# Performance work log

Hardware: AMD Instinct MI355X
Metric: run time of the kernel (lower is better)

## Reference

```python
import jax, jax.numpy as jnp
import numpy as np

N_NODES = 100000
N_EDGES = 1600000
IN_DIM, HID_DIM, OUT_DIM = 128, 128, 64


def setup_inputs() -> dict:
    key = jax.random.key(0)
    k1, k2, k3, k4, k5 = jax.random.split(key, 5)
    x = jax.random.normal(k1, (N_NODES, IN_DIM), dtype=jnp.float32)
    edge_index = jax.random.randint(k2, (2, N_EDGES), 0, N_NODES, dtype=jnp.int64)
    # PyG GCNConv linear weights (no bias); Glorot-ish scale for stability
    W1 = jax.random.normal(k3, (IN_DIM, HID_DIM), dtype=jnp.float32) * 0.05
    W2 = jax.random.normal(k4, (HID_DIM, HID_DIM), dtype=jnp.float32) * 0.05
    W3 = jax.random.normal(k5, (HID_DIM, OUT_DIM), dtype=jnp.float32) * 0.05
    return {"x": x, "edge_index": edge_index, "W1": W1, "W2": W2, "W3": W3}


def _gcn_conv(h, W, src, dst, num_nodes):
    # GCNConv(add_self_loops=False, normalize=False, bias=False):
    # linear transform, then scatter-add messages from src into dst
    msg = jnp.take(h @ W, src, axis=0)          # [E, d_out] gather
    return jax.ops.segment_sum(msg, dst, num_segments=num_nodes)  # [N, d_out]


def reference(x, edge_index, W1, W2, W3):
    num_nodes = x.shape[0]
    src, dst = edge_index[0], edge_index[1]
    h = jax.nn.relu(_gcn_conv(x, W1, src, dst, num_nodes))
    # dropout p=0.0 / eval mode -> identity
    h = jax.nn.relu(_gcn_conv(h, W2, src, dst, num_nodes))
    out = _gcn_conv(h, W3, src, dst, num_nodes)
    return jax.nn.log_softmax(out, axis=1)
```

## Files before the change

### kernel.cpp

```cpp
#include <hip/hip_runtime.h>
#include <hip/hip_bf16.h>

#define KDIM 128

typedef __attribute__((ext_vector_type(8))) __bf16 bf16x8;
typedef __attribute__((ext_vector_type(4))) float f32x4;
typedef __attribute__((ext_vector_type(2))) float f32x2;

static __device__ __forceinline__ unsigned short f2bf(float f) {
  unsigned u = __float_as_uint(f);
  u += 0x7fffu + ((u >> 16) & 1u);
  return (unsigned short)(u >> 16);
}
static __device__ __forceinline__ unsigned pack_bf16x2(float a, float b) {
  return (unsigned)f2bf(a) | ((unsigned)f2bf(b) << 16);
}
static __device__ __forceinline__ float2 unpack_bf16x2(unsigned u) {
  return make_float2(__uint_as_float(u << 16), __uint_as_float(u & 0xffff0000u));
}
static __device__ __forceinline__ unsigned relu2(unsigned u) {
  unsigned r = u;
  if (u & 0x00008000u) r &= 0xffff0000u;
  if (u & 0x80000000u) r &= 0x0000ffffu;
  return r;
}

static __device__ __forceinline__ unsigned char f2fp8(float f) {
#if __has_builtin(__builtin_amdgcn_cvt_pk_fp8_f32)
  return (unsigned char)(__builtin_amdgcn_cvt_pk_fp8_f32(f, f, 0, false) & 0xff);
#else
  unsigned s = (__float_as_uint(f) >> 24) & 0x80u;
  float a = fminf(fabsf(f), 448.f);
  if (a < 0.015625f) {
    unsigned m = (unsigned)(a * 512.f + 0.5f);
    return (unsigned char)(s | m);
  }
  unsigned v = __float_as_uint(a);
  v += 0x7ffffu + ((v >> 20) & 1u);
  unsigned em = (v >> 20) - 960u;
  if (em > 0x7eu) em = 0x7eu;
  return (unsigned char)(s | em);
#endif
}
static __device__ __forceinline__ float fp8dec(unsigned b) {
  unsigned s = (b & 0x80u) << 24;
  unsigned em = b & 0x7fu;
  float mag = (em >= 8) ? __uint_as_float((em + 960u) << 20)
                        : (float)em * 0.001953125f;
  return __uint_as_float(__float_as_uint(mag) | s);
}
static __device__ __forceinline__ float4 fp8x4_to_f32(unsigned u) {
#if __has_builtin(__builtin_amdgcn_cvt_pk_f32_fp8)
  f32x2 lo = __builtin_amdgcn_cvt_pk_f32_fp8(u, false);
  f32x2 hi = __builtin_amdgcn_cvt_pk_f32_fp8(u, true);
  return make_float4(lo[0], lo[1], hi[0], hi[1]);
#else
  return make_float4(fp8dec(u & 255u), fp8dec((u >> 8) & 255u),
                     fp8dec((u >> 16) & 255u), fp8dec(u >> 24));
#endif
}

__global__ __launch_bounds__(256) void wtrans_k(const float* __restrict__ W,
                                                unsigned short* __restrict__ Wt,
                                                int NOUT) {
  const int t = blockIdx.x * 256 + threadIdx.x;
  if (t >= NOUT * KDIM) return;
  const int n = t >> 7;
  const int k = t & 127;
  Wt[t] = f2bf(W[k * NOUT + n]);
}

template<int NOUT, bool AF32, bool RELU>
__global__ __launch_bounds__(512) void gemm_mfma_k(const void* __restrict__ Av,
                                                   const unsigned short* __restrict__ Wt,
                                                   unsigned char* __restrict__ C, int M) {
  constexpr int NT = NOUT / 16;
  __shared__ unsigned short Ws[NOUT][136];

  const int tid = threadIdx.x;
  for (int i = tid; i < NOUT * 16; i += 512) {
    const int n = i >> 4, k8 = i & 15;
    const uint4 v = *reinterpret_cast<const uint4*>(&Wt[n * KDIM + k8 * 8]);
    *reinterpret_cast<uint4*>(&Ws[n][k8 * 8]) = v;
  }

  const int wv = tid >> 6;
  const int l  = tid & 63;
  const int am = l & 15;
  const int kb = l >> 4;
  const int arow_g = blockIdx.x * 128 + wv * 16 + am;
  const bool valid = arow_g < M;
  const int arow = valid ? arow_g : 0;

  uint4 afr[4];
  if constexpr (AF32) {
    const float* A = (const float*)Av;
    #pragma unroll
    for (int ks = 0; ks < 4; ++ks) {
      const float4 lo = *reinterpret_cast<const float4*>(&A[(size_t)arow * 128 + ks * 32 + kb * 8]);
      const float4 hi = *reinterpret_cast<const float4*>(&A[(size_t)arow * 128 + ks * 32 + kb * 8 + 4]);
      afr[ks] = make_uint4(pack_bf16x2(lo.x, lo.y), pack_bf16x2(lo.z, lo.w),
                           pack_bf16x2(hi.x, hi.y), pack_bf16x2(hi.z, hi.w));
    }
  } else {
    const unsigned* A = (const unsigned*)Av;
    #pragma unroll
    for (int ks = 0; ks < 4; ++ks) {
      uint4 u = *reinterpret_cast<const uint4*>(&A[(size_t)arow * 64 + ks * 16 + kb * 4]);
      if constexpr (RELU) {
        u.x = relu2(u.x); u.y = relu2(u.y); u.z = relu2(u.z); u.w = relu2(u.w);
      }
      afr[ks] = u;
    }
  }
  if (!valid) {
    afr[0] = make_uint4(0, 0, 0, 0); afr[1] = afr[0];
    afr[2] = afr[0];                 afr[3] = afr[0];
  }

  f32x4 acc[NT];
  #pragma unroll
  for (int nt = 0; nt < NT; ++nt) {
    acc[nt][0] = 0.f; acc[nt][1] = 0.f; acc[nt][2] = 0.f; acc[nt][3] = 0.f;
  }

  __syncthreads();
  #pragma unroll
  for (int ks = 0; ks < 4; ++ks) {
    const bf16x8 a = __builtin_bit_cast(bf16x8, afr[ks]);
    #pragma unroll
    for (int nt = 0; nt < NT; ++nt) {
      const uint4 bv = *reinterpret_cast<const uint4*>(&Ws[nt * 16 + am][ks * 32 + kb * 8]);
      acc[nt] = __builtin_amdgcn_mfma_f32_16x16x32_bf16(
          a, __builtin_bit_cast(bf16x8, bv), acc[nt], 0, 0, 0);
    }
  }

  const int crow0 = blockIdx.x * 128 + wv * 16 + kb * 4;
  #pragma unroll
  for (int nt = 0; nt < NT; ++nt) {
    #pragma unroll
    for (int r = 0; r < 4; ++r) {
      const int rr = crow0 + r;
      if (rr < M) C[(size_t)rr * NOUT + nt * 16 + am] = f2fp8(acc[nt][r]);
    }
  }
}

__global__ __launch_bounds__(512) void hist_k(const int* __restrict__ dst,
                                              int* __restrict__ histT, int E) {
  __shared__ int h[256];
  if (threadIdx.x < 256) h[threadIdx.x] = 0;
  __syncthreads();
  for (int e = blockIdx.x * 512 + threadIdx.x; e < E; e += 256 * 512)
    atomicAdd(&h[dst[e] >> 9], 1);
  __syncthreads();
  if (threadIdx.x < 256) histT[threadIdx.x * 256 + blockIdx.x] = h[threadIdx.x];
}

__global__ __launch_bounds__(256) void scan1_k(const int* __restrict__ in,
                                               int* __restrict__ out,
                                               int* __restrict__ bsum, int N) {
  __shared__ int ls[256];
  const int t = threadIdx.x;
  const int base = blockIdx.x * 2048 + t * 8;
  int v[8];
  if (base + 8 <= N) {
    *reinterpret_cast<int4*>(&v[0]) = *reinterpret_cast<const int4*>(&in[base]);
    *reinterpret_cast<int4*>(&v[4]) = *reinterpret_cast<const int4*>(&in[base + 4]);
  } else {
    #pragma unroll
    for (int j = 0; j < 8; ++j) v[j] = (base + j < N) ? in[base + j] : 0;
  }
  int s = 0;
  #pragma unroll
  for (int j = 0; j < 8; ++j) { const int tmp = v[j]; v[j] = s; s += tmp; }
  int x = s;
  ls[t] = x;
  __syncthreads();
  for (int off = 1; off < 256; off <<= 1) {
    int y = 0;
    if (t >= off) y = ls[t - off];
    __syncthreads();
    x += y;
    ls[t] = x;
    __syncthreads();
  }
  const int excl = x - s;
  #pragma unroll
  for (int j = 0; j < 8; ++j)
    if (base + j < N) out[base + j] = excl + v[j];
  if (t == 255) bsum[blockIdx.x] = x;
}

__global__ __launch_bounds__(64) void scan2_k(const int* __restrict__ bsum,
                                              int* __restrict__ bscan, int NB) {
  const int t = threadIdx.x;
  const int v = (t < NB) ? bsum[t] : 0;
  int x = v;
  #pragma unroll
  for (int off = 1; off < 64; off <<= 1) {
    const int y = __shfl_up(x, off, 64);
    if (t >= off) x += y;
  }
  bscan[t] = x - v;
}

__global__ __launch_bounds__(256) void addoff_k(int* __restrict__ off,
                                                const int* __restrict__ bscan) {
  const int i = blockIdx.x * 256 + threadIdx.x;
  off[i] += bscan[i >> 11];
}

__global__ __launch_bounds__(512) void binscatter_k(const int* __restrict__ src,
                                                    const int* __restrict__ dst,
                                                    const int* __restrict__ histOff,
                                                    unsigned long long* __restrict__ epack,
                                                    int E) {
  __shared__ int cur[256];
  if (threadIdx.x < 256) cur[threadIdx.x] = histOff[threadIdx.x * 256 + blockIdx.x];
  __syncthreads();
  for (int e = blockIdx.x * 512 + threadIdx.x; e < E; e += 256 * 512) {
    const int d = dst[e], s = src[e];
    const int pos = atomicAdd(&cur[d >> 9], 1);
    epack[pos] = ((unsigned long long)(unsigned)d << 32) | (unsigned)s;
  }
}

__global__ __launch_bounds__(512) void binsort_k(const unsigned long long* __restrict__ epack,
                                                 const int* __restrict__ histOff,
                                                 int* __restrict__ rowptr,
                                                 int* __restrict__ col,
                                                 int N, int E) {
  __shared__ int hist[512];
  __shared__ int ls[256];
  __shared__ int cur[512];
  const int b = blockIdx.x;
  const int t = threadIdx.x;
  const int nbins = (N + 511) >> 9;
  const int beg = histOff[b * 256];
  const int end = (b + 1 < nbins) ? histOff[(b + 1) * 256] : E;

  hist[t] = 0;
  __syncthreads();
  for (int j = beg + t; j < end; j += 512)
    atomicAdd(&hist[(int)(epack[j] >> 32) & 511], 1);
  __syncthreads();

  int a = 0, b2 = 0, x = 0;
  if (t < 256) { a = hist[2 * t]; b2 = hist[2 * t + 1]; x = a + b2; ls[t] = x; }
  __syncthreads();
  for (int off = 1; off < 256; off <<= 1) {
    int y = 0;
    if (t < 256 && t >= off) y = ls[t - off];
    __syncthreads();
    if (t < 256) { x += y; ls[t] = x; }
    __syncthreads();
  }
  if (t < 256) {
    const int excl = x - a - b2;
    cur[2 * t] = excl;
    cur[2 * t + 1] = excl + a;
    const int g0 = b * 512 + 2 * t;
    if (g0 <= N) rowptr[g0] = beg + excl;
    if (g0 + 1 <= N) rowptr[g0 + 1] = beg + excl + a;
  }
  __syncthreads();
  for (int j = beg + t; j < end; j += 512) {
    const unsigned long long p = epack[j];
    const int d = (int)(p >> 32) & 511;
    const int s = (int)(p & 0xffffffffu);
    const int pos = atomicAdd(&cur[d], 1);
    col[beg + pos] = s;
  }
}

__global__ __launch_bounds__(256) void gather128_k(const unsigned* __restrict__ H32,
                                                   const int* __restrict__ rowptr,
                                                   const int* __restrict__ col,
                                                   unsigned* __restrict__ out, int N) {
  const int w = (int)((blockIdx.x * 256u + threadIdx.x) >> 6);
  const int lane = threadIdx.x & 63;
  const int h = lane >> 5;
  const int l5 = lane & 31;
  if (w >= N) return;
  const int beg = __builtin_amdgcn_readfirstlane(rowptr[w]);
  const int end = __builtin_amdgcn_readfirstlane(rowptr[w + 1]);

  float4 acc0 = make_float4(0.f, 0.f, 0.f, 0.f);
  float4 acc1 = make_float4(0.f, 0.f, 0.f, 0.f);
  float4 acc2 = make_float4(0.f, 0.f, 0.f, 0.f);
  float4 acc3 = make_float4(0.f, 0.f, 0.f, 0.f);

  int e = beg;
  for (; e + 8 <= end; e += 8) {
    const int sA = col[e + h];
    const int sB = col[e + 2 + h];
    const int sC = col[e + 4 + h];
    const int sD = col[e + 6 + h];
    const unsigned uA = H32[(size_t)sA * 32 + l5];
    const unsigned uB = H32[(size_t)sB * 32 + l5];
    const unsigned uC = H32[(size_t)sC * 32 + l5];
    const unsigned uD = H32[(size_t)sD * 32 + l5];
    const float4 vA = fp8x4_to_f32(uA), vB = fp8x4_to_f32(uB);
    const float4 vC = fp8x4_to_f32(uC), vD = fp8x4_to_f32(uD);
    acc0.x += vA.x; acc0.y += vA.y; acc0.z += vA.z; acc0.w += vA.w;
    acc1.x += vB.x; acc1.y += vB.y; acc1.z += vB.z; acc1.w += vB.w;
    acc2.x += vC.x; acc2.y += vC.y; acc2.z += vC.z; acc2.w += vC.w;
    acc3.x += vD.x; acc3.y += vD.y; acc3.z += vD.z; acc3.w += vD.w;
  }
  for (; e + 2 <= end; e += 2) {
    const float4 v = fp8x4_to_f32(H32[(size_t)col[e + h] * 32 + l5]);
    acc0.x += v.x; acc0.y += v.y; acc0.z += v.z; acc0.w += v.w;
  }
  if (e < end && h == 0) {
    const float4 v = fp8x4_to_f32(H32[(size_t)col[e] * 32 + l5]);
    acc1.x += v.x; acc1.y += v.y; acc1.z += v.z; acc1.w += v.w;
  }

  float4 a;
  a.x = (acc0.x + acc1.x) + (acc2.x + acc3.x);
  a.y = (acc0.y + acc1.y) + (acc2.y + acc3.y);
  a.z = (acc0.z + acc1.z) + (acc2.z + acc3.z);
  a.w = (acc0.w + acc1.w) + (acc2.w + acc3.w);
  a.x += __shfl_xor(a.x, 32, 64);
  a.y += __shfl_xor(a.y, 32, 64);
  a.z += __shfl_xor(a.z, 32, 64);
  a.w += __shfl_xor(a.w, 32, 64);

  if (h == 0) {
    *reinterpret_cast<uint2*>(&out[(size_t)w * 64 + l5 * 2]) =
        make_uint2(pack_bf16x2(a.x, a.y), pack_bf16x2(a.z, a.w));
  }
}

__global__ __launch_bounds__(256) void gather64lsm_k(const unsigned* __restrict__ H32,
                                                     const int* __restrict__ rowptr,
                                                     const int* __restrict__ col,
                                                     float* __restrict__ out, int N) {
  const int w = (int)((blockIdx.x * 256u + threadIdx.x) >> 6);
  const int lane = threadIdx.x & 63;
  const int q = lane >> 4;
  const int l4 = lane & 15;
  if (w >= N) return;
  const int beg = __builtin_amdgcn_readfirstlane(rowptr[w]);
  const int end = __builtin_amdgcn_readfirstlane(rowptr[w + 1]);

  float4 acc0 = make_float4(0.f, 0.f, 0.f, 0.f);
  float4 acc1 = make_float4(0.f, 0.f, 0.f, 0.f);

  int e = beg;
  for (; e + 8 <= end; e += 8) {
    const int s0 = col[e + q];
    const int s1 = col[e + 4 + q];
    const float4 v0 = fp8x4_to_f32(H32[(size_t)s0 * 16 + l4]);
    const float4 v1 = fp8x4_to_f32(H32[(size_t)s1 * 16 + l4]);
    acc0.x += v0.x; acc0.y += v0.y; acc0.z += v0.z; acc0.w += v0.w;
    acc1.x += v1.x; acc1.y += v1.y; acc1.z += v1.z; acc1.w += v1.w;
  }
  if (e + 4 <= end) {
    const float4 v = fp8x4_to_f32(H32[(size_t)col[e + q] * 16 + l4]);
    acc0.x += v.x; acc0.y += v.y; acc0.z += v.z; acc0.w += v.w;
    e += 4;
  }
  if (e + q < end) {
    const float4 v = fp8x4_to_f32(H32[(size_t)col[e + q] * 16 + l4]);
    acc1.x += v.x; acc1.y += v.y; acc1.z += v.z; acc1.w += v.w;
  }

  float4 a;
  a.x = acc0.x + acc1.x;
  a.y = acc0.y + acc1.y;
  a.z = acc0.z + acc1.z;
  a.w = acc0.w + acc1.w;
  a.x += __shfl_xor(a.x, 16, 64); a.x += __shfl_xor(a.x, 32, 64);
  a.y += __shfl_xor(a.y, 16, 64); a.y += __shfl_xor(a.y, 32, 64);
  a.z += __shfl_xor(a.z, 16, 64); a.z += __shfl_xor(a.z, 32, 64);
  a.w += __shfl_xor(a.w, 16, 64); a.w += __shfl_xor(a.w, 32, 64);

  float m = fmaxf(fmaxf(a.x, a.y), fmaxf(a.z, a.w));
  #pragma unroll
  for (int o = 8; o > 0; o >>= 1) m = fmaxf(m, __shfl_xor(m, o, 64));
  float s = __expf(a.x - m) + __expf(a.y - m) + __expf(a.z - m) + __expf(a.w - m);
  #pragma unroll
  for (int o = 8; o > 0; o >>= 1) s += __shfl_xor(s, o, 64);
  const float ls = __logf(s);

  if (lane < 16) {
    *reinterpret_cast<float4*>(&out[(size_t)w * 64 + l4 * 4]) =
        make_float4(a.x - m - ls, a.y - m - ls, a.z - m - ls, a.w - m - ls);
  }
}

extern "C" void kernel_launch(void* const* d_in, const int* in_sizes, int n_in,
                              void* d_out, int out_size, void* d_ws, size_t ws_size,
                              hipStream_t stream) {
  const float* x  = (const float*)d_in[0];
  const int*   ei = (const int*)d_in[1];
  const float* W1 = (const float*)d_in[2];
  const float* W2 = (const float*)d_in[3];
  const float* W3 = (const float*)d_in[4];
  float* out = (float*)d_out;

  const int N = in_sizes[0] / KDIM;
  const int E = in_sizes[1] / 2;
  const int* src = ei;
  const int* dst = ei + E;

  unsigned char* H = (unsigned char*)d_ws;
  unsigned* AGGp = (unsigned*)(H + (size_t)N * 128);
  unsigned short* Wt1 = (unsigned short*)(AGGp + (size_t)N * 64);
  unsigned short* Wt2 = Wt1 + 128 * 128;
  unsigned short* Wt3 = Wt2 + 128 * 128;
  int* col     = (int*)(Wt3 + 64 * 128);
  int* rowptr  = col + E;
  int* histT   = rowptr + (N + 8);
  int* histOff = histT + 65536;
  int* bsum2   = histOff + 65536;
  int* bscan2  = bsum2 + 64;
  unsigned long long* epack = (unsigned long long*)AGGp;

  const int nbins = (N + 511) / 512;

  wtrans_k<<<(128 * 128 + 255) / 256, 256, 0, stream>>>(W1, Wt1, 128);
  wtrans_k<<<(128 * 128 + 255) / 256, 256, 0, stream>>>(W2, Wt2, 128);
  wtrans_k<<<(64 * 128 + 255) / 256, 256, 0, stream>>>(W3, Wt3, 64);

  hist_k<<<256, 512, 0, stream>>>(dst, histT, E);
  scan1_k<<<32, 256, 0, stream>>>(histT, histOff, bsum2, 65536);
  scan2_k<<<1, 64, 0, stream>>>(bsum2, bscan2, 32);
  addoff_k<<<256, 256, 0, stream>>>(histOff, bscan2);
  binscatter_k<<<256, 512, 0, stream>>>(src, dst, histOff, epack, E);
  binsort_k<<<nbins, 512, 0, stream>>>(epack, histOff, rowptr, col, N, E);

  const int gemm_grid = (N + 127) / 128;
  const int gather_grid = (N + 3) / 4;

  gemm_mfma_k<128, true, false><<<gemm_grid, 512, 0, stream>>>(x, Wt1, H, N);
  gather128_k<<<gather_grid, 256, 0, stream>>>((const unsigned*)H, rowptr, col, AGGp, N);

  gemm_mfma_k<128, false, true><<<gemm_grid, 512, 0, stream>>>(AGGp, Wt2, H, N);
  gather128_k<<<gather_grid, 256, 0, stream>>>((const unsigned*)H, rowptr, col, AGGp, N);

  gemm_mfma_k<64, false, true><<<gemm_grid, 512, 0, stream>>>(AGGp, Wt3, H, N);
  gather64lsm_k<<<gather_grid, 256, 0, stream>>>((const unsigned*)H, rowptr, col, out, N);
}
```

Baseline: 232.7 us.

## Pack edges into 32-bit words, vectorize edge loads, deepen gather unrolling

```diff
diff --git a/kernel.cpp b/kernel.cpp
--- a/kernel.cpp
+++ b/kernel.cpp
@@ -152,8 +152,16 @@
   __shared__ int h[256];
   if (threadIdx.x < 256) h[threadIdx.x] = 0;
   __syncthreads();
-  for (int e = blockIdx.x * 512 + threadIdx.x; e < E; e += 256 * 512)
-    atomicAdd(&h[dst[e] >> 9], 1);
+  const int E4 = E >> 2;
+  for (int i = blockIdx.x * 512 + threadIdx.x; i < E4; i += 256 * 512) {
+    const int4 d4 = *reinterpret_cast<const int4*>(&dst[i * 4]);
+    atomicAdd(&h[d4.x >> 9], 1);
+    atomicAdd(&h[d4.y >> 9], 1);
+    atomicAdd(&h[d4.z >> 9], 1);
+    atomicAdd(&h[d4.w >> 9], 1);
+  }
+  if (blockIdx.x == 0 && threadIdx.x < (E & 3))
+    atomicAdd(&h[dst[E4 * 4 + threadIdx.x] >> 9], 1);
   __syncthreads();
   if (threadIdx.x < 256) histT[threadIdx.x * 256 + blockIdx.x] = h[threadIdx.x];
 }
@@ -215,19 +223,30 @@
 __global__ __launch_bounds__(512) void binscatter_k(const int* __restrict__ src,
                                                     const int* __restrict__ dst,
                                                     const int* __restrict__ histOff,
-                                                    unsigned long long* __restrict__ epack,
+                                                    unsigned* __restrict__ epack,
                                                     int E) {
   __shared__ int cur[256];
   if (threadIdx.x < 256) cur[threadIdx.x] = histOff[threadIdx.x * 256 + blockIdx.x];
   __syncthreads();
-  for (int e = blockIdx.x * 512 + threadIdx.x; e < E; e += 256 * 512) {
-    const int d = dst[e], s = src[e];
-    const int pos = atomicAdd(&cur[d >> 9], 1);
-    epack[pos] = ((unsigned long long)(unsigned)d << 32) | (unsigned)s;
-  }
-}
-
-__global__ __launch_bounds__(512) void binsort_k(const unsigned long long* __restrict__ epack,
+  const int E4 = E >> 2;
+  for (int i = blockIdx.x * 512 + threadIdx.x; i < E4; i += 256 * 512) {
+    const int4 d4 = *reinterpret_cast<const int4*>(&dst[i * 4]);
+    const int4 s4 = *reinterpret_cast<const int4*>(&src[i * 4]);
+    int p;
+    p = atomicAdd(&cur[d4.x >> 9], 1); epack[p] = ((unsigned)(d4.x & 511) << 17) | (unsigned)s4.x;
+    p = atomicAdd(&cur[d4.y >> 9], 1); epack[p] = ((unsigned)(d4.y & 511) << 17) | (unsigned)s4.y;
+    p = atomicAdd(&cur[d4.z >> 9], 1); epack[p] = ((unsigned)(d4.z & 511) << 17) | (unsigned)s4.z;
+    p = atomicAdd(&cur[d4.w >> 9], 1); epack[p] = ((unsigned)(d4.w & 511) << 17) | (unsigned)s4.w;
+  }
+  if (blockIdx.x == 0 && threadIdx.x < (E & 3)) {
+    const int e = E4 * 4 + threadIdx.x;
+    const int d = dst[e];
+    const int p = atomicAdd(&cur[d >> 9], 1);
+    epack[p] = ((unsigned)(d & 511) << 17) | (unsigned)src[e];
+  }
+}
+
+__global__ __launch_bounds__(512) void binsort_k(const unsigned* __restrict__ epack,
                                                  const int* __restrict__ histOff,
                                                  int* __restrict__ rowptr,
                                                  int* __restrict__ col,
@@ -244,7 +263,7 @@
   hist[t] = 0;
   __syncthreads();
   for (int j = beg + t; j < end; j += 512)
-    atomicAdd(&hist[(int)(epack[j] >> 32) & 511], 1);
+    atomicAdd(&hist[epack[j] >> 17], 1);
   __syncthreads();
 
   int a = 0, b2 = 0, x = 0;
@@ -267,11 +286,9 @@
   }
   __syncthreads();
   for (int j = beg + t; j < end; j += 512) {
-    const unsigned long long p = epack[j];
-    const int d = (int)(p >> 32) & 511;
-    const int s = (int)(p & 0xffffffffu);
-    const int pos = atomicAdd(&cur[d], 1);
-    col[beg + pos] = s;
+    const unsigned p = epack[j];
+    const int pos = atomicAdd(&cur[p >> 17], 1);
+    col[beg + pos] = (int)(p & 0x1ffffu);
   }
 }
 
@@ -293,21 +310,47 @@
   float4 acc3 = make_float4(0.f, 0.f, 0.f, 0.f);
 
   int e = beg;
+  for (; e + 16 <= end; e += 16) {
+    const int s0 = col[e + h];
+    const int s1 = col[e + 2 + h];
+    const int s2 = col[e + 4 + h];
+    const int s3 = col[e + 6 + h];
+    const int s4 = col[e + 8 + h];
+    const int s5 = col[e + 10 + h];
+    const int s6 = col[e + 12 + h];
+    const int s7 = col[e + 14 + h];
+    const unsigned u0 = H32[(size_t)s0 * 32 + l5];
+    const unsigned u1 = H32[(size_t)s1 * 32 + l5];
+    const unsigned u2 = H32[(size_t)s2 * 32 + l5];
+    const unsigned u3 = H32[(size_t)s3 * 32 + l5];
+    const unsigned u4 = H32[(size_t)s4 * 32 + l5];
+    const unsigned u5 = H32[(size_t)s5 * 32 + l5];
+    const unsigned u6 = H32[(size_t)s6 * 32 + l5];
+    const unsigned u7 = H32[(size_t)s7 * 32 + l5];
+    float4 v;
+    v = fp8x4_to_f32(u0); acc0.x += v.x; acc0.y += v.y; acc0.z += v.z; acc0.w += v.w;
+    v = fp8x4_to_f32(u1); acc1.x += v.x; acc1.y += v.y; acc1.z += v.z; acc1.w += v.w;
+    v = fp8x4_to_f32(u2); acc2.x += v.x; acc2.y += v.y; acc2.z += v.z; acc2.w += v.w;
+    v = fp8x4_to_f32(u3); acc3.x += v.x; acc3.y += v.y; acc3.z += v.z; acc3.w += v.w;
+    v = fp8x4_to_f32(u4); acc0.x += v.x; acc0.y += v.y; acc0.z += v.z; acc0.w += v.w;
+    v = fp8x4_to_f32(u5); acc1.x += v.x; acc1.y += v.y; acc1.z += v.z; acc1.w += v.w;
+    v = fp8x4_to_f32(u6); acc2.x += v.x; acc2.y += v.y; acc2.z += v.z; acc2.w += v.w;
+    v = fp8x4_to_f32(u7); acc3.x += v.x; acc3.y += v.y; acc3.z += v.z; acc3.w += v.w;
+  }
   for (; e + 8 <= end; e += 8) {
-    const int sA = col[e + h];
-    const int sB = col[e + 2 + h];
-    const int sC = col[e + 4 + h];
-    const int sD = col[e + 6 + h];
-    const unsigned uA = H32[(size_t)sA * 32 + l5];
-    const unsigned uB = H32[(size_t)sB * 32 + l5];
-    const unsigned uC = H32[(size_t)sC * 32 + l5];
-    const unsigned uD = H32[(size_t)sD * 32 + l5];
-    const float4 vA = fp8x4_to_f32(uA), vB = fp8x4_to_f32(uB);
-    const float4 vC = fp8x4_to_f32(uC), vD = fp8x4_to_f32(uD);
-    acc0.x += vA.x; acc0.y += vA.y; acc0.z += vA.z; acc0.w += vA.w;
-    acc1.x += vB.x; acc1.y += vB.y; acc1.z += vB.z; acc1.w += vB.w;
-    acc2.x += vC.x; acc2.y += vC.y; acc2.z += vC.z; acc2.w += vC.w;
-    acc3.x += vD.x; acc3.y += vD.y; acc3.z += vD.z; acc3.w += vD.w;
+    const int s0 = col[e + h];
+    const int s1 = col[e + 2 + h];
+    const int s2 = col[e + 4 + h];
+    const int s3 = col[e + 6 + h];
+    const unsigned u0 = H32[(size_t)s0 * 32 + l5];
+    const unsigned u1 = H32[(size_t)s1 * 32 + l5];
+    const unsigned u2 = H32[(size_t)s2 * 32 + l5];
+    const unsigned u3 = H32[(size_t)s3 * 32 + l5];
+    float4 v;
+    v = fp8x4_to_f32(u0); acc0.x += v.x; acc0.y += v.y; acc0.z += v.z; acc0.w += v.w;
+    v = fp8x4_to_f32(u1); acc1.x += v.x; acc1.y += v.y; acc1.z += v.z; acc1.w += v.w;
+    v = fp8x4_to_f32(u2); acc2.x += v.x; acc2.y += v.y; acc2.z += v.z; acc2.w += v.w;
+    v = fp8x4_to_f32(u3); acc3.x += v.x; acc3.y += v.y; acc3.z += v.z; acc3.w += v.w;
   }
   for (; e + 2 <= end; e += 2) {
     const float4 v = fp8x4_to_f32(H32[(size_t)col[e + h] * 32 + l5]);
@@ -350,6 +393,21 @@
   float4 acc1 = make_float4(0.f, 0.f, 0.f, 0.f);
 
   int e = beg;
+  for (; e + 16 <= end; e += 16) {
+    const int s0 = col[e + q];
+    const int s1 = col[e + 4 + q];
+    const int s2 = col[e + 8 + q];
+    const int s3 = col[e + 12 + q];
+    const unsigned u0 = H32[(size_t)s0 * 16 + l4];
+    const unsigned u1 = H32[(size_t)s1 * 16 + l4];
+    const unsigned u2 = H32[(size_t)s2 * 16 + l4];
+    const unsigned u3 = H32[(size_t)s3 * 16 + l4];
+    float4 v;
+    v = fp8x4_to_f32(u0); acc0.x += v.x; acc0.y += v.y; acc0.z += v.z; acc0.w += v.w;
+    v = fp8x4_to_f32(u1); acc1.x += v.x; acc1.y += v.y; acc1.z += v.z; acc1.w += v.w;
+    v = fp8x4_to_f32(u2); acc0.x += v.x; acc0.y += v.y; acc0.z += v.z; acc0.w += v.w;
+    v = fp8x4_to_f32(u3); acc1.x += v.x; acc1.y += v.y; acc1.z += v.z; acc1.w += v.w;
+  }
   for (; e + 8 <= end; e += 8) {
     const int s0 = col[e + q];
     const int s1 = col[e + 4 + q];
@@ -418,7 +476,7 @@
   int* histOff = histT + 65536;
   int* bsum2   = histOff + 65536;
   int* bscan2  = bsum2 + 64;
-  unsigned long long* epack = (unsigned long long*)AGGp;
+  unsigned* epack = (unsigned*)AGGp;
 
   const int nbins = (N + 511) / 512;
 
```

After: 221.7 us. 1.05x faster.
